# Optimization experiments

Hardware: AMD Instinct MI355X
Metric: run time of the kernel (lower is better)

Reference implementation:

```python
import jax, jax.numpy as jnp
import numpy as np

SUP = 7
EPS = 1e-12

def _gather(t, idx):
    # t: (b, v, d), idx: (b, v, n) -> (b, v, n, d)
    return jax.vmap(lambda tb, ib: tb[ib])(t, idx)

def _knn(v, k):
    # squared pairwise distance, exclude self (smallest), return k neighbors
    q = jnp.sum(v * v, axis=-1)
    d = q[:, :, None] + q[:, None, :] - 2.0 * jnp.einsum('bid,bjd->bij', v, v)
    _, idx = jax.lax.top_k(-d, k + 1)
    return idx[:, :, 1:]

def _dir_norm(v, idx):
    d = _gather(v, idx) - v[:, :, None, :]
    n = jnp.sqrt(jnp.sum(d * d, axis=-1, keepdims=True))
    return d / jnp.maximum(n, EPS)

def _col_norm(d):
    n = jnp.sqrt(jnp.sum(d * d, axis=0, keepdims=True))
    return d / jnp.maximum(n, EPS)

def _conv_surface(idx, v, directions, kernel_num):
    theta = jax.nn.silu(_dir_norm(v, idx) @ _col_norm(directions))  # (b,V,n,SUP*K)
    b, V, n, _ = theta.shape
    theta = theta.reshape(b, V, n, SUP, kernel_num)
    return jnp.sum(jnp.max(theta, axis=2), axis=2)

def _conv_layer(idx, v, fm, W, bias, directions, out_c):
    b, V, n = idx.shape
    theta = jax.nn.silu(_dir_norm(v, idx) @ _col_norm(directions))  # (b,V,n,SUP*out_c)
    feat = fm @ W + bias                                             # (b,V,(SUP+1)*out_c)
    center = feat[:, :, :out_c]
    support = _gather(feat[:, :, out_c:], idx)                       # (b,V,n,SUP*out_c)
    act = (theta * support).reshape(b, V, n, SUP, out_c)
    act = jnp.sum(jnp.max(act, axis=2), axis=2)
    return center + act

def _bn(x, g, b, eps=1e-5):
    # BatchNorm1d in training mode: stats over batch and vertex dims
    m = jnp.mean(x, axis=(0, 1))
    var = jnp.var(x, axis=(0, 1))
    return (x - m) / jnp.sqrt(var + eps) * g + b

def _nearest(target, source):
    d = (jnp.sum(source * source, -1)[:, None, :] + jnp.sum(target * target, -1)[:, :, None]
         - 2.0 * jnp.einsum('bid,bjd->bij', target, source))
    return jnp.argmin(d, axis=-1)  # (b, v1)

def _forward(x, d0, w1, b1, dir1, g1, bb1, w2, b2, dir2, g2, bb2,
             w3, b3, dir3, g3, bb3, w4, b4, dir4, perm1, perm2):
    nb = _knn(x, 10)
    fm0 = jax.nn.silu(_conv_surface(nb, x, d0, 128))
    fm1 = jax.nn.silu(_bn(_conv_layer(nb, x, fm0, w1, b1, dir1, 128), g1, bb1))
    # pool 1: max over 4-NN features, then subsample to V/4
    pooled = jnp.max(_gather(fm1, _knn(x, 4)), axis=2)
    v1 = x[:, perm1]
    f1 = pooled[:, perm1]
    nb = _knn(v1, 10)
    fm2 = jax.nn.silu(_bn(_conv_layer(nb, v1, f1, w2, b2, dir2, 256), g2, bb2))
    fm3 = jax.nn.silu(_bn(_conv_layer(nb, v1, fm2, w3, b3, dir3, 256), g3, bb3))
    # pool 2
    pooled = jnp.max(_gather(fm3, _knn(v1, 4)), axis=2)
    v2 = v1[:, perm2]
    f2 = pooled[:, perm2]
    nb = _knn(v2, 10)
    fm4 = _conv_layer(nb, v2, f2, w4, b4, dir4, 512)
    n1 = _nearest(x, v1)
    n2 = _nearest(x, v2)
    up = lambda f, i: jax.vmap(lambda fb, ib: fb[ib])(f, i)
    return jnp.concatenate([fm0, fm1, up(fm2, n1), up(fm3, n1), up(fm4, n2)], axis=-1)

def setup_inputs() -> dict:
    key = jax.random.key(0)
    ks = jax.random.split(key, 24)
    B, V = 2, 4096
    uni = lambda k, shape, s: jax.random.uniform(k, shape, jnp.float32, -s, s)
    s1 = (128 * (SUP + 1)) ** -0.5
    s2 = (256 * (SUP + 1)) ** -0.5
    s4 = (512 * (SUP + 1)) ** -0.5
    s0 = (SUP * 128) ** -0.5
    inp = {
        'x': jax.random.normal(ks[0], (B, V, 3), jnp.float32),
        'd0': uni(ks[1], (3, SUP * 128), s0),
        'w1': uni(ks[2], (128, (SUP + 1) * 128), s1),
        'b1': uni(ks[3], ((SUP + 1) * 128,), s1),
        'dir1': uni(ks[4], (3, SUP * 128), s1),
        'g1': jnp.ones((128,), jnp.float32),
        'bb1': jnp.zeros((128,), jnp.float32),
        'w2': uni(ks[5], (128, (SUP + 1) * 256), s2),
        'b2': uni(ks[6], ((SUP + 1) * 256,), s2),
        'dir2': uni(ks[7], (3, SUP * 256), s2),
        'g2': jnp.ones((256,), jnp.float32),
        'bb2': jnp.zeros((256,), jnp.float32),
        'w3': uni(ks[8], (256, (SUP + 1) * 256), s2),
        'b3': uni(ks[9], ((SUP + 1) * 256,), s2),
        'dir3': uni(ks[10], (3, SUP * 256), s2),
        'g3': jnp.ones((256,), jnp.float32),
        'bb3': jnp.zeros((256,), jnp.float32),
        'w4': uni(ks[11], (256, (SUP + 1) * 512), s4),
        'b4': uni(ks[12], ((SUP + 1) * 512,), s4),
        'dir4': uni(ks[13], (3, SUP * 512), s4),
        'perm1': jax.random.permutation(ks[20], V)[: V // 4].astype(jnp.int32),
        'perm2': jax.random.permutation(ks[21], V // 4)[: V // 16].astype(jnp.int32),
    }
    return inp

def reference(x, d0, w1, b1, dir1, g1, bb1, w2, b2, dir2, g2, bb2,
              w3, b3, dir3, g3, bb3, w4, b4, dir4, perm1, perm2):
    return _forward(x, d0, w1, b1, dir1, g1, bb1, w2, b2, dir2, g2, bb2,
                    w3, b3, dir3, g3, bb3, w4, b4, dir4, perm1, perm2)
```

## Files before the change

kernel.cpp:

```cpp
#include <hip/hip_runtime.h>
#include <math.h>
#include <float.h>
#include <limits.h>

#define BNUM 2
#define V0 4096
#define V1N 1024
#define V2N 256
#define SUPN 7

typedef float float4v __attribute__((ext_vector_type(4)));
typedef float float2v __attribute__((ext_vector_type(2)));
typedef unsigned short ushort4v __attribute__((ext_vector_type(4)));
typedef unsigned long long u64;

__device__ __forceinline__ float fast_silu(float x){
  return __fdividef(x, 1.0f + __expf(-x));
}

__device__ __forceinline__ unsigned short f2bf(float f){
  unsigned int u=__float_as_uint(f);
  u += 0x7FFFu + ((u>>16)&1u);
  return (unsigned short)(u>>16);
}
__device__ __forceinline__ float bf2f(unsigned short h){
  return __uint_as_float(((unsigned int)h)<<16);
}

__device__ __forceinline__ unsigned int fkey(float f){
  unsigned int u = __float_as_uint(f);
  int m = ((int)u) >> 31;
  return u ^ (unsigned int)(m | 0x80000000);
}

__device__ __forceinline__ u64 shfl_xor_u64(u64 v, int m){
  unsigned int lo = (unsigned int)v, hi = (unsigned int)(v>>32);
  lo = (unsigned int)__shfl_xor((int)lo, m);
  hi = (unsigned int)__shfl_xor((int)hi, m);
  return ((u64)hi<<32) | lo;
}

__global__ void colnorm_all_k(const float* __restrict__ d0, const float* __restrict__ dir1,
                              const float* __restrict__ dir2, const float* __restrict__ dir3,
                              const float* __restrict__ dir4,
                              float* __restrict__ cn0, float* __restrict__ cn1,
                              float* __restrict__ cn2, float* __restrict__ cn3,
                              float* __restrict__ cn4, float* __restrict__ stats){
  int c = blockIdx.x*256 + threadIdx.x;
  if(c < 1280) stats[c] = 0.0f;
  const float* s; float* o; int nc;
  if(c < 896){ s=d0; o=cn0; nc=896; }
  else if((c-=896) < 896){ s=dir1; o=cn1; nc=896; }
  else if((c-=896) < 1792){ s=dir2; o=cn2; nc=1792; }
  else if((c-=1792) < 1792){ s=dir3; o=cn3; nc=1792; }
  else { c-=1792; if(c>=3584) return; s=dir4; o=cn4; nc=3584; }
  float a=s[c], b=s[nc+c], e=s[2*nc+c];
  float n=sqrtf(a*a+b*b+e*e); n=fmaxf(n,1e-12f);
  o[c]=a/n; o[nc+c]=b/n; o[2*nc+c]=e/n;
}

template<int VC, int THREADS, int MINW>
__global__ __launch_bounds__(THREADS, MINW) void knn10_k(const float* __restrict__ pts,
    int* __restrict__ out_idx, float* __restrict__ out_dirn)
{
  constexpr int CHUNK = VC/64;
  constexpr int QPB = THREADS/64;
  __shared__ float4v sp4[VC];
  __shared__ float sdd[QPB][34];
  __shared__ int   sdi[QPB][34];
  int t = threadIdx.x;
  int lane = t & 63;
  int wv   = t >> 6;
  int b = blockIdx.y;
  int j = blockIdx.x*QPB + wv;
  const float* pb = pts + (size_t)b*VC*3;
  for(int i=t; i<VC; i+=THREADS){
    float x=pb[3*i], y=pb[3*i+1], z=pb[3*i+2];
    float4v v; v[0]=x; v[1]=y; v[2]=z; v[3]=x*x+y*y+z*z;
    sp4[i]=v;
  }
  __syncthreads();
  float qx=pb[3*j], qy=pb[3*j+1], qz=pb[3*j+2];
  float qs=qx*qx+qy*qy+qz*qz;

  float dc[CHUNK];
  float p0=INFINITY, p1=INFINITY, p2=INFINITY, p3=INFINITY;
  #pragma unroll
  for(int c=0;c<CHUNK;c++){
    float4v p = sp4[c*64+lane];
    float dot = qx*p[0]+qy*p[1]+qz*p[2];
    float d = fmaf(-2.0f, dot, p[3]+qs);
    dc[c]=d;
    float s=d, a;
    a=fminf(p0,s); s=fmaxf(p0,s); p0=a;
    a=fminf(p1,s); s=fmaxf(p1,s); p1=a;
    a=fminf(p2,s); s=fmaxf(p2,s); p2=a;
    p3=fminf(p3,s);
  }

  float prev=-INFINITY;
  for(int sel=0; sel<11; ++sel){
    float cand = p0>prev ? p0 : (p1>prev ? p1 : (p2>prev ? p2 : (p3>prev ? p3 : INFINITY)));
    #pragma unroll
    for(int s=32;s;s>>=1) cand = fminf(cand, __shfl_xor(cand, s));
    prev=cand;
  }
  float v11 = prev;

  int cnt=0;
  #pragma unroll
  for(int c=0;c<CHUNK;c++){
    bool hit = dc[c] <= v11;
    u64 m = __ballot(hit);
    if(m){
      if(hit){
        int pos = cnt + __popcll(m & ((1ull<<lane)-1ull));
        if(pos<32){ sdd[wv][pos]=dc[c]; sdi[wv][pos]=c*64+lane; }
      }
      cnt += (int)__popcll(m);
    }
  }
  if(cnt>32) cnt=32;

  if(lane < cnt){
    float dl = sdd[wv][lane]; int il = sdi[wv][lane];
    int rank=0;
    for(int m2=0;m2<cnt;m2++){
      float dm=sdd[wv][m2]; int im=sdi[wv][m2];
      rank += (dm<dl || (dm==dl && im<il)) ? 1 : 0;
    }
    if(rank>=1 && rank<=10){
      size_t obase=((size_t)b*VC+j)*10 + (rank-1);
      out_idx[obase]=il;
      float4v p = sp4[il];
      float dx=p[0]-qx, dy=p[1]-qy, dz=p[2]-qz;
      float n=sqrtf(dx*dx+dy*dy+dz*dz); n=fmaxf(n,1e-12f);
      out_dirn[obase*3]=dx/n; out_dirn[obase*3+1]=dy/n; out_dirn[obase*3+2]=dz/n;
    }
  }
}

__global__ __launch_bounds__(512) void nearest_both_k(
    const float* __restrict__ v1, const float* __restrict__ v2,
    const float* __restrict__ x,
    int* __restrict__ n1, int* __restrict__ n2)
{
  __shared__ float4v s1[V1N];
  __shared__ float4v s2[V2N];
  int t=threadIdx.x;
  int lane=t&63, wv=t>>6;
  int b=blockIdx.y; int j=blockIdx.x*8+wv;
  const float* c1=v1+(size_t)b*V1N*3;
  const float* c2=v2+(size_t)b*V2N*3;
  for(int i=t;i<V1N;i+=512){
    float xx=c1[3*i],yy=c1[3*i+1],zz=c1[3*i+2];
    float4v v; v[0]=xx;v[1]=yy;v[2]=zz;v[3]=xx*xx+yy*yy+zz*zz; s1[i]=v;
  }
  for(int i=t;i<V2N;i+=512){
    float xx=c2[3*i],yy=c2[3*i+1],zz=c2[3*i+2];
    float4v v; v[0]=xx;v[1]=yy;v[2]=zz;v[3]=xx*xx+yy*yy+zz*zz; s2[i]=v;
  }
  __syncthreads();
  const float* qb=x+(size_t)b*V0*3;
  float qx=qb[3*j],qy=qb[3*j+1],qz=qb[3*j+2];
  float qs=qx*qx+qy*qy+qz*qz;
  u64 bk=~0ull;
  #pragma unroll 4
  for(int c=0;c<V1N/64;c++){
    int i=c*64+lane;
    float4v p=s1[i];
    float dot=qx*p[0]+qy*p[1]+qz*p[2];
    float d=fmaf(-2.0f,dot,p[3]+qs);
    u64 k=((u64)fkey(d)<<32)|(unsigned int)i;
    bk = k<bk ? k : bk;
  }
  #pragma unroll
  for(int s=32;s;s>>=1){ u64 o=shfl_xor_u64(bk,s); bk = o<bk?o:bk; }
  if(lane==0) n1[(size_t)b*V0+j]=(int)(bk&0xffffffffu);
  bk=~0ull;
  #pragma unroll 4
  for(int c=0;c<V2N/64;c++){
    int i=c*64+lane;
    float4v p=s2[i];
    float dot=qx*p[0]+qy*p[1]+qz*p[2];
    float d=fmaf(-2.0f,dot,p[3]+qs);
    u64 k=((u64)fkey(d)<<32)|(unsigned int)i;
    bk = k<bk ? k : bk;
  }
  #pragma unroll
  for(int s=32;s;s>>=1){ u64 o=shfl_xor_u64(bk,s); bk = o<bk?o:bk; }
  if(lane==0) n2[(size_t)b*V0+j]=(int)(bk&0xffffffffu);
}

template<int NODES>
__global__ __launch_bounds__(64*NODES) void conv_surf_k(
    const float* __restrict__ dirn, const float* __restrict__ cnd,
    float* __restrict__ fm0, float* __restrict__ outbuf)
{
  int tid=threadIdx.x, nd=tid>>6, t=tid&63;
  int b=blockIdx.y, i=blockIdx.x*NODES+nd;
  __shared__ float sd[NODES][32];
  if(t<30) sd[nd][t]=dirn[((size_t)(b*V0+i))*30+t];
  __syncthreads();
  float acc0=0.0f, acc1=0.0f;
  for(int s=0;s<SUPN;s++){
    int col=s*128+t;
    float wa0=cnd[col],     wa1=cnd[896+col],     wa2=cnd[1792+col];
    float wb0=cnd[col+64],  wb1=cnd[896+col+64],  wb2=cnd[1792+col+64];
    float m0=-INFINITY, m1=-INFINITY;
    #pragma unroll
    for(int n=0;n<10;n++){
      float dx=sd[nd][3*n], dy=sd[nd][3*n+1], dz=sd[nd][3*n+2];
      m0=fmaxf(m0, fast_silu(dx*wa0+dy*wa1+dz*wa2));
      m1=fmaxf(m1, fast_silu(dx*wb0+dy*wb1+dz*wb2));
    }
    acc0+=m0; acc1+=m1;
  }
  float r0=fast_silu(acc0), r1=fast_silu(acc1);
  size_t frow=(size_t)(b*V0+i)*128;
  fm0[frow+t]=r0; fm0[frow+64+t]=r1;
  size_t orow=(size_t)(b*V0+i)*1280;
  outbuf[orow+t]=r0; outbuf[orow+64+t]=r1;
}

__global__ __launch_bounds__(256) void gemm_split_k(
    const float* __restrict__ A, const float* __restrict__ W,
    const float* __restrict__ bias,
    float* __restrict__ Cc, unsigned short* __restrict__ Sp,
    int M, int N, int K, int outC)
{
  __shared__ float As[16][132];
  __shared__ float Bs[16][132];
  int t=threadIdx.x;
  int tx=t&15, ty=t>>4;
  int bm=blockIdx.y*128, bn=blockIdx.x*128;
  float4v acc[2][2][4];
  #pragma unroll
  for(int a=0;a<2;a++)
    #pragma unroll
    for(int bidx=0;bidx<2;bidx++)
      #pragma unroll
      for(int m=0;m<4;m++) acc[a][bidx][m]=(float4v)(0.0f);
  int arow=t>>2, akk=(t&3)*4;
  int brow=t>>4, bcol=(t&15)*4;
  const float* Aa=&A[(size_t)(bm+arow)*K    + akk];
  const float* Ab=&A[(size_t)(bm+64+arow)*K + akk];
  const float* Wa=&W[(size_t)brow*N + bn+bcol];
  const float* Wb=&W[(size_t)brow*N + bn+64+bcol];
  float4v a0=*(const float4v*)Aa;
  float4v a1=*(const float4v*)Ab;
  float4v b0=*(const float4v*)Wa;
  float4v b1=*(const float4v*)Wb;
  for(int k0=0;k0<K;k0+=16){
    __syncthreads();
    #pragma unroll
    for(int u=0;u<4;u++){ As[akk+u][arow]=a0[u]; As[akk+u][64+arow]=a1[u]; }
    *(float4v*)&Bs[brow][bcol]=b0;
    *(float4v*)&Bs[brow][64+bcol]=b1;
    __syncthreads();
    if(k0+16<K){
      a0=*(const float4v*)(Aa + k0+16);
      a1=*(const float4v*)(Ab + k0+16);
      b0=*(const float4v*)(Wa + (size_t)(k0+16)*N);
      b1=*(const float4v*)(Wb + (size_t)(k0+16)*N);
    }
    #pragma unroll
    for(int kk=0;kk<16;kk++){
      float4v alo=*(const float4v*)&As[kk][ty*4];
      float4v ahi=*(const float4v*)&As[kk][64+ty*4];
      float4v blo=*(const float4v*)&Bs[kk][tx*4];
      float4v bhi=*(const float4v*)&Bs[kk][64+tx*4];
      #pragma unroll
      for(int mi=0;mi<4;mi++){
        acc[0][0][mi] += alo[mi]*blo;
        acc[0][1][mi] += alo[mi]*bhi;
        acc[1][0][mi] += ahi[mi]*blo;
        acc[1][1][mi] += ahi[mi]*bhi;
      }
    }
  }
  float4v bl=*(const float4v*)&bias[bn+tx*4];
  float4v bh=*(const float4v*)&bias[bn+64+tx*4];
  if(bn + 128 <= outC){
    #pragma unroll
    for(int mh=0;mh<2;mh++)
      #pragma unroll
      for(int mi=0;mi<4;mi++){
        size_t row=(size_t)(bm+mh*64+ty*4+mi);
        *(float4v*)&Cc[row*outC + bn+tx*4]    = acc[mh][0][mi]+bl;
        *(float4v*)&Cc[row*outC + bn+64+tx*4] = acc[mh][1][mi]+bh;
      }
  } else {
    int sw = 7*outC;
    int scol = bn - outC;
    #pragma unroll
    for(int mh=0;mh<2;mh++)
      #pragma unroll
      for(int mi=0;mi<4;mi++){
        size_t row=(size_t)(bm+mh*64+ty*4+mi);
        float4v r0=acc[mh][0][mi]+bl, r1=acc[mh][1][mi]+bh;
        ushort4v p0,p1;
        #pragma unroll
        for(int u=0;u<4;u++){ p0[u]=f2bf(r0[u]); p1[u]=f2bf(r1[u]); }
        *(ushort4v*)&Sp[row*sw + scol+tx*4]    = p0;
        *(ushort4v*)&Sp[row*sw + scol+64+tx*4] = p1;
      }
  }
}

template<int C, int TPN, int NODES>
__global__ __launch_bounds__(TPN*NODES) void conv_agg_k(
    const float* __restrict__ cent, const unsigned short* __restrict__ sup,
    int Vb,
    const float* __restrict__ dirn, const int* __restrict__ nbidx,
    const float* __restrict__ cnd,
    float* __restrict__ outp, float* __restrict__ stats)
{
  constexpr int ncol = SUPN*C;
  constexpr int NT = TPN*NODES;
  int tid=threadIdx.x, nd=tid/TPN, t=tid%TPN;
  int b=blockIdx.y, i=blockIdx.x*NODES+nd;
  __shared__ float sd[NODES][32];
  __shared__ int snb[NODES][12];
  __shared__ float ssum[C], ssq[C];
  __shared__ float scn[3*ncol];
  if(t<30) sd[nd][t]=dirn[((size_t)(b*Vb+i))*30+t];
  if(t<10) snb[nd][t]=nbidx[(size_t)(b*Vb+i)*10+t];
  for(int c=tid;c<3*ncol;c+=NT) scn[c]=cnd[c];
  if(stats) for(int c=tid;c<C;c+=NT){ ssum[c]=0.0f; ssq[c]=0.0f; }
  __syncthreads();

  const int col0 = t*4;
  const unsigned short* fb = sup + (size_t)b*Vb*ncol;

  float m[SUPN][4];
  #pragma unroll
  for(int s=0;s<SUPN;s++)
    #pragma unroll
    for(int v=0;v<4;v++) m[s][v]=-INFINITY;

  ushort4v bufA[SUPN], bufB[SUPN];
  float dax,day,daz, dbx,dby,dbz;
  {
    unsigned int off=(unsigned int)snb[nd][0]*ncol + col0;
    #pragma unroll
    for(int s=0;s<SUPN;s++) bufA[s]=*(const ushort4v*)&fb[off + s*C];
    dax=sd[nd][0]; day=sd[nd][1]; daz=sd[nd][2];
  }
  #pragma unroll 1
  for(int np=0;np<5;np++){
    {
      int nn=2*np+1;
      unsigned int off=(unsigned int)snb[nd][nn]*ncol + col0;
      #pragma unroll
      for(int s=0;s<SUPN;s++) bufB[s]=*(const ushort4v*)&fb[off + s*C];
      dbx=sd[nd][3*nn]; dby=sd[nd][3*nn+1]; dbz=sd[nd][3*nn+2];
    }
    #pragma unroll
    for(int s=0;s<SUPN;s++){
      int cb=s*C+col0;
      float4v w0=*(const float4v*)&scn[cb];
      float4v w1=*(const float4v*)&scn[ncol+cb];
      float4v w2=*(const float4v*)&scn[2*ncol+cb];
      ushort4v sv=bufA[s];
      #pragma unroll
      for(int v=0;v<4;v++){
        float d = dax*w0[v] + day*w1[v] + daz*w2[v];
        m[s][v] = fmaxf(m[s][v], fast_silu(d)*bf2f(sv[v]));
      }
    }
    if(np<4){
      int nn=2*np+2;
      unsigned int off=(unsigned int)snb[nd][nn]*ncol + col0;
      #pragma unroll
      for(int s=0;s<SUPN;s++) bufA[s]=*(const ushort4v*)&fb[off + s*C];
      dax=sd[nd][3*nn]; day=sd[nd][3*nn+1]; daz=sd[nd][3*nn+2];
    }
    #pragma unroll
    for(int s=0;s<SUPN;s++){
      int cb=s*C+col0;
      float4v w0=*(const float4v*)&scn[cb];
      float4v w1=*(const float4v*)&scn[ncol+cb];
      float4v w2=*(const float4v*)&scn[2*ncol+cb];
      ushort4v sv=bufB[s];
      #pragma unroll
      for(int v=0;v<4;v++){
        float d = dbx*w0[v] + dby*w1[v] + dbz*w2[v];
        m[s][v] = fmaxf(m[s][v], fast_silu(d)*bf2f(sv[v]));
      }
    }
  }

  float acc[4];
  {
    float4v cv=*(const float4v*)&cent[(size_t)(b*Vb+i)*C + col0];
    #pragma unroll
    for(int v=0;v<4;v++){
      acc[v]=cv[v];
      #pragma unroll
      for(int s=0;s<SUPN;s++) acc[v]+=m[s][v];
    }
  }
  {
    float4v ov;
    #pragma unroll
    for(int v=0;v<4;v++) ov[v]=acc[v];
    *(float4v*)&outp[(size_t)(b*Vb+i)*C + col0]=ov;
  }
  if(stats){
    #pragma unroll
    for(int v=0;v<4;v++){
      atomicAdd(&ssum[col0+v], acc[v]);
      atomicAdd(&ssq[col0+v], acc[v]*acc[v]);
    }
    __syncthreads();
    for(int c=tid;c<C;c+=NT){
      atomicAdd(&stats[c], ssum[c]);
      atomicAdd(&stats[C+c], ssq[c]);
    }
  }
}

__global__ void bn_silu_k(const float* __restrict__ xin, const float* __restrict__ sums,
                          float invM, int C, const float* __restrict__ g, const float* __restrict__ bb,
                          float* __restrict__ y, int nquad, float* __restrict__ osl, int cshift)
{
  int gid=blockIdx.x*blockDim.x+threadIdx.x;
  if(gid>=nquad) return;
  int base=gid*4;
  int c=base&(C-1);
  float4v xv=*(const float4v*)&xin[base];
  float4v sm=*(const float4v*)&sums[c];
  float4v sq=*(const float4v*)&sums[C+c];
  float4v gv=*(const float4v*)&g[c];
  float4v bv=*(const float4v*)&bb[c];
  float4v r;
  #pragma unroll
  for(int u=0;u<4;u++){
    float mean=sm[u]*invM;
    float var=sq[u]*invM - mean*mean;
    float v=(xv[u]-mean)*rsqrtf(var+1e-5f)*gv[u]+bv[u];
    r[u]=fast_silu(v);
  }
  *(float4v*)&y[base]=r;
  if(osl){
    int row=base>>cshift;
    *(float4v*)&osl[(size_t)row*1280 + c]=r;
  }
}

template<int C, int NODES>
__global__ __launch_bounds__((C/4)*NODES) void pool_gather_k(
    const float* __restrict__ fm, int Vsrc,
    const int* __restrict__ idx10, const int* __restrict__ perm,
    const float* __restrict__ vsrc,
    float* __restrict__ fout, float* __restrict__ vout, int Vq)
{
  constexpr int TPN=C/4;
  int tid=threadIdx.x, nd=tid/TPN, t=tid%TPN;
  int b=blockIdx.y, j=blockIdx.x*NODES+nd;
  int r=perm[j];
  const int* id=idx10+((size_t)b*Vsrc+r)*10;
  const float* fb=fm+(size_t)b*Vsrc*C;
  float4v m=(float4v)(-INFINITY);
  #pragma unroll
  for(int n=0;n<4;n++){
    float4v fv=*(const float4v*)&fb[(size_t)id[n]*C + t*4];
    #pragma unroll
    for(int u=0;u<4;u++) m[u]=fmaxf(m[u],fv[u]);
  }
  *(float4v*)&fout[(size_t)(b*Vq+j)*C + t*4]=m;
  if(t<3) vout[((size_t)b*Vq+j)*3+t]=vsrc[((size_t)b*Vsrc+r)*3+t];
}

__global__ __launch_bounds__(256) void concat_k(
    const float* __restrict__ fm2, const float* __restrict__ fm3,
    const float* __restrict__ fm4,
    const int* __restrict__ n1, const int* __restrict__ n2,
    float* __restrict__ outp)
{
  int b=blockIdx.y, i=blockIdx.x, t=threadIdx.x;
  int j1=n1[b*V0+i], j2=n2[b*V0+i];
  float4v v;
  if(t<64)       v = ((const float4v*)(fm2 + ((size_t)b*V1N+j1)*256))[t];
  else if(t<128) v = ((const float4v*)(fm3 + ((size_t)b*V1N+j1)*256))[t-64];
  else           v = ((const float4v*)(fm4 + ((size_t)b*V2N+j2)*512))[t-128];
  ((float4v*)(outp + (size_t)(b*V0+i)*1280))[64+t] = v;
}

extern "C" void kernel_launch(void* const* d_in, const int* in_sizes, int n_in,
                              void* d_out, int out_size, void* d_ws, size_t ws_size,
                              hipStream_t stream) {
  const float* x   =(const float*)d_in[0];
  const float* d0  =(const float*)d_in[1];
  const float* w1  =(const float*)d_in[2];
  const float* b1  =(const float*)d_in[3];
  const float* dir1=(const float*)d_in[4];
  const float* g1  =(const float*)d_in[5];
  const float* bb1 =(const float*)d_in[6];
  const float* w2  =(const float*)d_in[7];
  const float* b2  =(const float*)d_in[8];
  const float* dir2=(const float*)d_in[9];
  const float* g2  =(const float*)d_in[10];
  const float* bb2 =(const float*)d_in[11];
  const float* w3  =(const float*)d_in[12];
  const float* b3  =(const float*)d_in[13];
  const float* dir3=(const float*)d_in[14];
  const float* g3  =(const float*)d_in[15];
  const float* bb3 =(const float*)d_in[16];
  const float* w4  =(const float*)d_in[17];
  const float* b4  =(const float*)d_in[18];
  const float* dir4=(const float*)d_in[19];
  const int* perm1 =(const int*)d_in[20];
  const int* perm2 =(const int*)d_in[21];
  float* out=(float*)d_out;

  float* w=(float*)d_ws;
  size_t off=0;
  auto alloc=[&](size_t n){ float* p=w+off; off+=n; return p; };
  float* cn0 =alloc(2688);
  float* cn1 =alloc(2688);
  float* cn2 =alloc(5376);
  float* cn3 =alloc(5376);
  float* cn4 =alloc(10752);
  float* dirnx =alloc((size_t)BNUM*V0*30);
  float* dirnv1=alloc((size_t)BNUM*V1N*30);
  float* dirnv2=alloc((size_t)BNUM*V2N*30);
  float* fm0 =alloc((size_t)BNUM*V0*128);
  float* cent=alloc((size_t)BNUM*V0*128);
  unsigned short* supb=(unsigned short*)alloc((size_t)BNUM*V0*896/2);
  float* fm1r=alloc((size_t)BNUM*V0*128);
  float* fm1 =alloc((size_t)BNUM*V0*128);
  float* f1  =alloc((size_t)BNUM*V1N*128);
  float* v1  =alloc((size_t)BNUM*V1N*3);
  float* fm2r=alloc((size_t)BNUM*V1N*256);
  float* fm2 =alloc((size_t)BNUM*V1N*256);
  float* fm3r=alloc((size_t)BNUM*V1N*256);
  float* fm3 =alloc((size_t)BNUM*V1N*256);
  float* f2  =alloc((size_t)BNUM*V2N*256);
  float* v2  =alloc((size_t)BNUM*V2N*3);
  float* fm4 =alloc((size_t)BNUM*V2N*512);
  float* stats=alloc(1280);
  int* idx10x =(int*)alloc((size_t)BNUM*V0*10);
  int* idx10v1=(int*)alloc((size_t)BNUM*V1N*10);
  int* idx10v2=(int*)alloc((size_t)BNUM*V2N*10);
  int* n1i =(int*)alloc((size_t)BNUM*V0);
  int* n2i =(int*)alloc((size_t)BNUM*V0);

  colnorm_all_k<<<dim3(35),256,0,stream>>>(d0,dir1,dir2,dir3,dir4,cn0,cn1,cn2,cn3,cn4,stats);

  knn10_k<V0,1024,4><<<dim3(V0/16,BNUM),1024,0,stream>>>(x, idx10x, dirnx);
  conv_surf_k<4><<<dim3(V0/4,BNUM),256,0,stream>>>(dirnx, cn0, fm0, out);

  gemm_split_k<<<dim3(1024/128,(BNUM*V0)/128),256,0,stream>>>(fm0, w1, b1, cent, supb, BNUM*V0, 1024, 128, 128);
  conv_agg_k<128,32,8><<<dim3(V0/8,BNUM),256,0,stream>>>(cent, supb, V0, dirnx, idx10x, cn1, fm1r, stats);
  bn_silu_k<<<dim3((BNUM*V0*128/4)/256),256,0,stream>>>(fm1r, stats, 1.0f/(BNUM*V0), 128, g1, bb1, fm1, BNUM*V0*128/4, out+128, 7);

  pool_gather_k<128,8><<<dim3(V1N/8,BNUM),256,0,stream>>>(fm1, V0, idx10x, perm1, x, f1, v1, V1N);

  knn10_k<V1N,256,6><<<dim3(V1N/4,BNUM),256,0,stream>>>(v1, idx10v1, dirnv1);

  gemm_split_k<<<dim3(2048/128,(BNUM*V1N)/128),256,0,stream>>>(f1, w2, b2, cent, supb, BNUM*V1N, 2048, 128, 256);
  conv_agg_k<256,64,4><<<dim3(V1N/4,BNUM),256,0,stream>>>(cent, supb, V1N, dirnv1, idx10v1, cn2, fm2r, stats+256);
  bn_silu_k<<<dim3((BNUM*V1N*256/4)/256),256,0,stream>>>(fm2r, stats+256, 1.0f/(BNUM*V1N), 256, g2, bb2, fm2, BNUM*V1N*256/4, nullptr, 8);

  gemm_split_k<<<dim3(2048/128,(BNUM*V1N)/128),256,0,stream>>>(fm2, w3, b3, cent, supb, BNUM*V1N, 2048, 256, 256);
  conv_agg_k<256,64,4><<<dim3(V1N/4,BNUM),256,0,stream>>>(cent, supb, V1N, dirnv1, idx10v1, cn3, fm3r, stats+768);
  bn_silu_k<<<dim3((BNUM*V1N*256/4)/256),256,0,stream>>>(fm3r, stats+768, 1.0f/(BNUM*V1N), 256, g3, bb3, fm3, BNUM*V1N*256/4, nullptr, 8);

  pool_gather_k<256,4><<<dim3(V2N/4,BNUM),256,0,stream>>>(fm3, V1N, idx10v1, perm2, v1, f2, v2, V2N);

  knn10_k<V2N,256,6><<<dim3(V2N/4,BNUM),256,0,stream>>>(v2, idx10v2, dirnv2);

  gemm_split_k<<<dim3(4096/128,(BNUM*V2N)/128),256,0,stream>>>(f2, w4, b4, cent, supb, BNUM*V2N, 4096, 256, 512);
  conv_agg_k<512,128,2><<<dim3(V2N/2,BNUM),256,0,stream>>>(cent, supb, V2N, dirnv2, idx10v2, cn4, fm4, nullptr);

  nearest_both_k<<<dim3(V0/8,BNUM),512,0,stream>>>(v1, v2, x, n1i, n2i);

  concat_k<<<dim3(V0,BNUM),256,0,stream>>>(fm2, fm3, fm4, n1i, n2i, out);
}
```

Baseline: 479.6 us.

## Split conv aggregation support slices across two thread groups per node

Each conv_agg_k block now runs two thread groups over the same nodes. One group handles support slices 0-3 and the other slices 4-6, and the partial sums are combined through shared memory. Blocks cover half as many nodes, so the grid doubles. The aim is to cut per-thread register pressure (fewer max accumulators and prefetch buffers) and add parallelism in the latency-bound gather. In exchange it adds a block barrier and shared-memory traffic, and each block loads the column-normalized directions for fewer nodes.

Result: slower. 495.7 us (+3.3%).

```diff
diff --git a/kernel.cpp b/kernel.cpp
--- a/kernel.cpp
+++ b/kernel.cpp
@@ -308,8 +308,81 @@
   }
 }
 
+template<int C, int NS, int S0>
+__device__ __forceinline__ void agg_slice(
+    const unsigned short* __restrict__ fb,
+    const float* sdn, const int* snbn, const float* scn,
+    int col0, float acc[4])
+{
+  constexpr int ncol = SUPN*C;
+  float m[NS][4];
+  #pragma unroll
+  for(int s=0;s<NS;s++)
+    #pragma unroll
+    for(int v=0;v<4;v++) m[s][v]=-INFINITY;
+
+  ushort4v bufA[NS], bufB[NS];
+  float dax,day,daz, dbx,dby,dbz;
+  {
+    unsigned int off=(unsigned int)snbn[0]*ncol + col0;
+    #pragma unroll
+    for(int s=0;s<NS;s++) bufA[s]=*(const ushort4v*)&fb[off + (S0+s)*C];
+    dax=sdn[0]; day=sdn[1]; daz=sdn[2];
+  }
+  #pragma unroll 1
+  for(int np=0;np<5;np++){
+    {
+      int nn=2*np+1;
+      unsigned int off=(unsigned int)snbn[nn]*ncol + col0;
+      #pragma unroll
+      for(int s=0;s<NS;s++) bufB[s]=*(const ushort4v*)&fb[off + (S0+s)*C];
+      dbx=sdn[3*nn]; dby=sdn[3*nn+1]; dbz=sdn[3*nn+2];
+    }
+    #pragma unroll
+    for(int s=0;s<NS;s++){
+      int cb=(S0+s)*C+col0;
+      float4v w0=*(const float4v*)&scn[cb];
+      float4v w1=*(const float4v*)&scn[ncol+cb];
+      float4v w2=*(const float4v*)&scn[2*ncol+cb];
+      ushort4v sv=bufA[s];
+      #pragma unroll
+      for(int v=0;v<4;v++){
+        float d = dax*w0[v] + day*w1[v] + daz*w2[v];
+        m[s][v] = fmaxf(m[s][v], fast_silu(d)*bf2f(sv[v]));
+      }
+    }
+    if(np<4){
+      int nn=2*np+2;
+      unsigned int off=(unsigned int)snbn[nn]*ncol + col0;
+      #pragma unroll
+      for(int s=0;s<NS;s++) bufA[s]=*(const ushort4v*)&fb[off + (S0+s)*C];
+      dax=sdn[3*nn]; day=sdn[3*nn+1]; daz=sdn[3*nn+2];
+    }
+    #pragma unroll
+    for(int s=0;s<NS;s++){
+      int cb=(S0+s)*C+col0;
+      float4v w0=*(const float4v*)&scn[cb];
+      float4v w1=*(const float4v*)&scn[ncol+cb];
+      float4v w2=*(const float4v*)&scn[2*ncol+cb];
+      ushort4v sv=bufB[s];
+      #pragma unroll
+      for(int v=0;v<4;v++){
+        float d = dbx*w0[v] + dby*w1[v] + dbz*w2[v];
+        m[s][v] = fmaxf(m[s][v], fast_silu(d)*bf2f(sv[v]));
+      }
+    }
+  }
+  #pragma unroll
+  for(int v=0;v<4;v++){
+    float a=m[0][v];
+    #pragma unroll
+    for(int s=1;s<NS;s++) a+=m[s][v];
+    acc[v]=a;
+  }
+}
+
 template<int C, int TPN, int NODES>
-__global__ __launch_bounds__(TPN*NODES) void conv_agg_k(
+__global__ __launch_bounds__(2*TPN*NODES) void conv_agg_k(
     const float* __restrict__ cent, const unsigned short* __restrict__ sup,
     int Vb,
     const float* __restrict__ dirn, const int* __restrict__ nbidx,
@@ -317,15 +390,20 @@
     float* __restrict__ outp, float* __restrict__ stats)
 {
   constexpr int ncol = SUPN*C;
-  constexpr int NT = TPN*NODES;
-  int tid=threadIdx.x, nd=tid/TPN, t=tid%TPN;
+  constexpr int GSZ = TPN*NODES;
+  constexpr int NT = 2*GSZ;
+  int tid=threadIdx.x;
+  int grp=tid/GSZ, rr=tid%GSZ, nd=rr/TPN, t=rr%TPN;
   int b=blockIdx.y, i=blockIdx.x*NODES+nd;
   __shared__ float sd[NODES][32];
   __shared__ int snb[NODES][12];
   __shared__ float ssum[C], ssq[C];
   __shared__ float scn[3*ncol];
-  if(t<30) sd[nd][t]=dirn[((size_t)(b*Vb+i))*30+t];
-  if(t<10) snb[nd][t]=nbidx[(size_t)(b*Vb+i)*10+t];
+  __shared__ float pacc[NODES][C];
+  if(grp==0){
+    if(t<30) sd[nd][t]=dirn[((size_t)(b*Vb+i))*30+t];
+    if(t<10) snb[nd][t]=nbidx[(size_t)(b*Vb+i)*10+t];
+  }
   for(int c=tid;c<3*ncol;c+=NT) scn[c]=cnd[c];
   if(stats) for(int c=tid;c<C;c+=NT){ ssum[c]=0.0f; ssq[c]=0.0f; }
   __syncthreads();
@@ -333,86 +411,37 @@
   const int col0 = t*4;
   const unsigned short* fb = sup + (size_t)b*Vb*ncol;
 
-  float m[SUPN][4];
-  #pragma unroll
-  for(int s=0;s<SUPN;s++)
-    #pragma unroll
-    for(int v=0;v<4;v++) m[s][v]=-INFINITY;
-
-  ushort4v bufA[SUPN], bufB[SUPN];
-  float dax,day,daz, dbx,dby,dbz;
-  {
-    unsigned int off=(unsigned int)snb[nd][0]*ncol + col0;
-    #pragma unroll
-    for(int s=0;s<SUPN;s++) bufA[s]=*(const ushort4v*)&fb[off + s*C];
-    dax=sd[nd][0]; day=sd[nd][1]; daz=sd[nd][2];
-  }
-  #pragma unroll 1
-  for(int np=0;np<5;np++){
-    {
-      int nn=2*np+1;
-      unsigned int off=(unsigned int)snb[nd][nn]*ncol + col0;
-      #pragma unroll
-      for(int s=0;s<SUPN;s++) bufB[s]=*(const ushort4v*)&fb[off + s*C];
-      dbx=sd[nd][3*nn]; dby=sd[nd][3*nn+1]; dbz=sd[nd][3*nn+2];
-    }
-    #pragma unroll
-    for(int s=0;s<SUPN;s++){
-      int cb=s*C+col0;
-      float4v w0=*(const float4v*)&scn[cb];
-      float4v w1=*(const float4v*)&scn[ncol+cb];
-      float4v w2=*(const float4v*)&scn[2*ncol+cb];
-      ushort4v sv=bufA[s];
+  float acc[4];
+  if(grp==1){
+    agg_slice<C,3,4>(fb, &sd[nd][0], &snb[nd][0], scn, col0, acc);
+    float4v pv;
+    #pragma unroll
+    for(int v=0;v<4;v++) pv[v]=acc[v];
+    *(float4v*)&pacc[nd][col0]=pv;
+  } else {
+    agg_slice<C,4,0>(fb, &sd[nd][0], &snb[nd][0], scn, col0, acc);
+  }
+  __syncthreads();
+
+  if(grp==0){
+    float4v cv=*(const float4v*)&cent[(size_t)(b*Vb+i)*C + col0];
+    float4v pv=*(const float4v*)&pacc[nd][col0];
+    float tot[4];
+    #pragma unroll
+    for(int v=0;v<4;v++) tot[v]=cv[v]+acc[v]+pv[v];
+    float4v ov;
+    #pragma unroll
+    for(int v=0;v<4;v++) ov[v]=tot[v];
+    *(float4v*)&outp[(size_t)(b*Vb+i)*C + col0]=ov;
+    if(stats){
       #pragma unroll
       for(int v=0;v<4;v++){
-        float d = dax*w0[v] + day*w1[v] + daz*w2[v];
-        m[s][v] = fmaxf(m[s][v], fast_silu(d)*bf2f(sv[v]));
+        atomicAdd(&ssum[col0+v], tot[v]);
+        atomicAdd(&ssq[col0+v], tot[v]*tot[v]);
       }
     }
-    if(np<4){
-      int nn=2*np+2;
-      unsigned int off=(unsigned int)snb[nd][nn]*ncol + col0;
-      #pragma unroll
-      for(int s=0;s<SUPN;s++) bufA[s]=*(const ushort4v*)&fb[off + s*C];
-      dax=sd[nd][3*nn]; day=sd[nd][3*nn+1]; daz=sd[nd][3*nn+2];
-    }
-    #pragma unroll
-    for(int s=0;s<SUPN;s++){
-      int cb=s*C+col0;
-      float4v w0=*(const float4v*)&scn[cb];
-      float4v w1=*(const float4v*)&scn[ncol+cb];
-      float4v w2=*(const float4v*)&scn[2*ncol+cb];
-      ushort4v sv=bufB[s];
-      #pragma unroll
-      for(int v=0;v<4;v++){
-        float d = dbx*w0[v] + dby*w1[v] + dbz*w2[v];
-        m[s][v] = fmaxf(m[s][v], fast_silu(d)*bf2f(sv[v]));
-      }
-    }
-  }
-
-  float acc[4];
-  {
-    float4v cv=*(const float4v*)&cent[(size_t)(b*Vb+i)*C + col0];
-    #pragma unroll
-    for(int v=0;v<4;v++){
-      acc[v]=cv[v];
-      #pragma unroll
-      for(int s=0;s<SUPN;s++) acc[v]+=m[s][v];
-    }
-  }
-  {
-    float4v ov;
-    #pragma unroll
-    for(int v=0;v<4;v++) ov[v]=acc[v];
-    *(float4v*)&outp[(size_t)(b*Vb+i)*C + col0]=ov;
   }
   if(stats){
-    #pragma unroll
-    for(int v=0;v<4;v++){
-      atomicAdd(&ssum[col0+v], acc[v]);
-      atomicAdd(&ssq[col0+v], acc[v]*acc[v]);
-    }
     __syncthreads();
     for(int c=tid;c<C;c+=NT){
       atomicAdd(&stats[c], ssum[c]);
@@ -553,7 +582,7 @@
   conv_surf_k<4><<<dim3(V0/4,BNUM),256,0,stream>>>(dirnx, cn0, fm0, out);
 
   gemm_split_k<<<dim3(1024/128,(BNUM*V0)/128),256,0,stream>>>(fm0, w1, b1, cent, supb, BNUM*V0, 1024, 128, 128);
-  conv_agg_k<128,32,8><<<dim3(V0/8,BNUM),256,0,stream>>>(cent, supb, V0, dirnx, idx10x, cn1, fm1r, stats);
+  conv_agg_k<128,32,4><<<dim3(V0/4,BNUM),256,0,stream>>>(cent, supb, V0, dirnx, idx10x, cn1, fm1r, stats);
   bn_silu_k<<<dim3((BNUM*V0*128/4)/256),256,0,stream>>>(fm1r, stats, 1.0f/(BNUM*V0), 128, g1, bb1, fm1, BNUM*V0*128/4, out+128, 7);
 
   pool_gather_k<128,8><<<dim3(V1N/8,BNUM),256,0,stream>>>(fm1, V0, idx10x, perm1, x, f1, v1, V1N);
@@ -561,11 +590,11 @@
   knn10_k<V1N,256,6><<<dim3(V1N/4,BNUM),256,0,stream>>>(v1, idx10v1, dirnv1);
 
   gemm_split_k<<<dim3(2048/128,(BNUM*V1N)/128),256,0,stream>>>(f1, w2, b2, cent, supb, BNUM*V1N, 2048, 128, 256);
-  conv_agg_k<256,64,4><<<dim3(V1N/4,BNUM),256,0,stream>>>(cent, supb, V1N, dirnv1, idx10v1, cn2, fm2r, stats+256);
+  conv_agg_k<256,64,2><<<dim3(V1N/2,BNUM),256,0,stream>>>(cent, supb, V1N, dirnv1, idx10v1, cn2, fm2r, stats+256);
   bn_silu_k<<<dim3((BNUM*V1N*256/4)/256),256,0,stream>>>(fm2r, stats+256, 1.0f/(BNUM*V1N), 256, g2, bb2, fm2, BNUM*V1N*256/4, nullptr, 8);
 
   gemm_split_k<<<dim3(2048/128,(BNUM*V1N)/128),256,0,stream>>>(fm2, w3, b3, cent, supb, BNUM*V1N, 2048, 256, 256);
-  conv_agg_k<256,64,4><<<dim3(V1N/4,BNUM),256,0,stream>>>(cent, supb, V1N, dirnv1, idx10v1, cn3, fm3r, stats+768);
+  conv_agg_k<256,64,2><<<dim3(V1N/2,BNUM),256,0,stream>>>(cent, supb, V1N, dirnv1, idx10v1, cn3, fm3r, stats+768);
   bn_silu_k<<<dim3((BNUM*V1N*256/4)/256),256,0,stream>>>(fm3r, stats+768, 1.0f/(BNUM*V1N), 256, g3, bb3, fm3, BNUM*V1N*256/4, nullptr, 8);
 
   pool_gather_k<256,4><<<dim3(V2N/4,BNUM),256,0,stream>>>(fm3, V1N, idx10v1, perm2, v1, f2, v2, V2N);
@@ -573,7 +602,7 @@
   knn10_k<V2N,256,6><<<dim3(V2N/4,BNUM),256,0,stream>>>(v2, idx10v2, dirnv2);
 
   gemm_split_k<<<dim3(4096/128,(BNUM*V2N)/128),256,0,stream>>>(f2, w4, b4, cent, supb, BNUM*V2N, 4096, 256, 512);
-  conv_agg_k<512,128,2><<<dim3(V2N/2,BNUM),256,0,stream>>>(cent, supb, V2N, dirnv2, idx10v2, cn4, fm4, nullptr);
+  conv_agg_k<512,128,1><<<dim3(V2N,BNUM),256,0,stream>>>(cent, supb, V2N, dirnv2, idx10v2, cn4, fm4, nullptr);
 
   nearest_both_k<<<dim3(V0/8,BNUM),512,0,stream>>>(v1, v2, x, n1i, n2i);
 
```
